# Kernel tuning notes

Measured on AMD Instinct MI355X. Metric: run time of the kernel, lower is better.

Reference implementation:

```python
import jax, jax.numpy as jnp
import numpy as np

NUM_EMBEDDINGS = 4096
EMBEDDING_DIM = 256
COMMITMENT_COST = 0.25


def setup_inputs() -> dict:
    key = jax.random.key(0)
    k1, k2 = jax.random.split(key)
    x = jax.random.normal(k1, (64, 32, 32, EMBEDDING_DIM), dtype=jnp.float32)
    # torch init: uniform(-1/K, 1/K)
    codebook = jax.random.uniform(
        k2, (NUM_EMBEDDINGS, EMBEDDING_DIM), dtype=jnp.float32,
        minval=-1.0 / NUM_EMBEDDINGS, maxval=1.0 / NUM_EMBEDDINGS)
    return {"x": x, "codebook": codebook}


def reference(x, codebook):
    D = codebook.shape[1]
    flat_x = x.reshape(-1, D)                                   # [N, D]
    distances = (jnp.sum(flat_x ** 2, axis=1, keepdims=True)
                 + jnp.sum(codebook ** 2, axis=1)
                 - 2.0 * flat_x @ codebook.T)                   # [N, K]
    encoding_indices = jnp.argmin(distances, axis=1)            # [N]
    quantized = codebook[encoding_indices].reshape(x.shape)     # gather (== one-hot matmul)
    q_sg = jax.lax.stop_gradient(quantized)
    x_sg = jax.lax.stop_gradient(x)
    commitment_loss = jnp.mean((q_sg - x) ** 2)
    codebook_loss = jnp.mean((quantized - x_sg) ** 2)
    vq_loss = codebook_loss + COMMITMENT_COST * commitment_loss
    # straight-through estimator
    quantized_st = x + jax.lax.stop_gradient(quantized - x)
    return quantized_st, vq_loss
```

## Files before the change

### kernel.cpp

```cpp
#include <hip/hip_runtime.h>
#include <stdint.h>

#define DIM     256
#define NCODES  4096
#define NROWS   65536
#define ROWS_WG 128
#define CCOLS   64
#define NCH     (NCODES / CCOLS)
#define CHB     (CCOLS * DIM)

#define OFF_BIMG  0u
#define OFF_HC    (1u << 20)

typedef __attribute__((ext_vector_type(8)))  int   i32x8;
typedef __attribute__((ext_vector_type(16))) float f32x16;
typedef const __attribute__((address_space(1))) uint32_t* gas1_t;
typedef __attribute__((address_space(3))) uint32_t*       las3_t;

__device__ __forceinline__ uint32_t pk4(float a, float b, float c, float d) {
  uint32_t lo = (uint32_t)__builtin_amdgcn_cvt_pk_fp8_f32(a, b, 0, false) & 0xFFFFu;
  uint32_t hi = (uint32_t)__builtin_amdgcn_cvt_pk_fp8_f32(c, d, 0, false) & 0xFFFFu;
  return lo | (hi << 16);
}

__global__ __launch_bounds__(256) void k1_prep(const float* __restrict__ cb,
                                               uint8_t* __restrict__ ws,
                                               float* __restrict__ out,
                                               int out_size) {
  const int t = threadIdx.x;
  if (blockIdx.x == 0 && t == 0) out[out_size - 1] = 0.0f;
  const int code = blockIdx.x * 4 + (t >> 6);
  const int l = t & 63;
  float4 v = ((const float4*)(cb + (size_t)code * DIM))[l];
  float ax = v.x * 4096.0f, ay = v.y * 4096.0f;
  float az = v.z * 4096.0f, aw = v.w * 4096.0f;
  uint32_t off = (uint32_t)(code >> 6) * (uint32_t)CHB
               + (uint32_t)(l >> 2) * 1024u
               + (uint32_t)(code & 63) * 16u + (uint32_t)(l & 3) * 4u;
  *(uint32_t*)(ws + OFF_BIMG + off) = pk4(ax, ay, az, aw);
  float s = ax * ax + ay * ay + az * az + aw * aw;
  #pragma unroll
  for (int m = 1; m < 64; m <<= 1) s += __shfl_xor(s, m, 64);
  if (l == 0) ((float*)(ws + OFF_HC))[code] = 512.0f + s * (1.0f / 8192.0f);
}

__global__ __launch_bounds__(256, 2) void k2_argmin(const float* __restrict__ x,
                                                    const float* __restrict__ cb,
                                                    uint8_t* __restrict__ ws,
                                                    float* __restrict__ out,
                                                    int out_size) {
  __shared__ uint4 smem4[4096];
  char* smem = (char*)&smem4[0];
  const int t = threadIdx.x;
  const int wave = t >> 6;
  const int lane = t & 63;
  const int c = lane & 31;
  const int g = lane >> 5;
  const int wg = blockIdx.x;
  const uint8_t* __restrict__ Bimg = ws + OFF_BIMG;
  const float* __restrict__ hcg = (const float*)(ws + OFF_HC);

  const int rbw = (wave >> 1) * 64;
  const int cbw = (wave & 1) * 32;

  const float* xb = x + (size_t)wg * ROWS_WG * DIM;
  {
    #pragma unroll
    for (int it = 0; it < 16; ++it) {
      int u = it * 256 + t;
      int row = u >> 5;
      int k8 = u & 31;
      const float4* src = (const float4*)(xb + (size_t)row * DIM + k8 * 8);
      float4 v0 = src[0], v1 = src[1];
      uint32_t* d = (uint32_t*)(smem + (k8 >> 2) * 4096 + row * 32 + (k8 & 3) * 8);
      d[0] = pk4(-v0.x, -v0.y, -v0.z, -v0.w);
      d[1] = pk4(-v1.x, -v1.y, -v1.z, -v1.w);
    }
  }
  __syncthreads();

  i32x8 a[2][4];
  #pragma unroll
  for (int rt = 0; rt < 2; ++rt)
    #pragma unroll
    for (int ks = 0; ks < 4; ++ks)
      a[rt][ks] = *(const i32x8*)(smem + (ks * 2 + g) * 4096
                                  + (rbw + rt * 32 + c) * 32);
  __syncthreads();

  char* wbuf = smem + wave * 16384;
  auto stageW = [&](int buf, int ch) {
    const uint8_t* gs = Bimg + (size_t)ch * CHB + (size_t)g * 1024
                      + (size_t)(cbw + c) * 16;
    char* lb = wbuf + buf * 8192;
    #pragma unroll
    for (int p = 0; p < 8; ++p)
      __builtin_amdgcn_global_load_lds((gas1_t)(uintptr_t)(gs + p * 2048),
                                       (las3_t)(uintptr_t)(lb + p * 1024),
                                       16, 0, 0);
  };

  uint32_t key[2][16];
  #pragma unroll
  for (int rt = 0; rt < 2; ++rt)
    #pragma unroll
    for (int r = 0; r < 16; ++r) key[rt][r] = 0xFFFFFFFFu;

  const int hoff = cbw + c;
  const uint32_t maskhi = 0xFFFFF000u;

  const int ch0 = ((wg * 7) + ((wg >> 8) * 29)) & 63;

  stageW(0, ch0);
  float h_cur = hcg[ch0 * CCOLS + hoff];

  for (int i = 0; i < NCH; ++i) {
    const int cur = i & 1;
    const int ch = (ch0 + i) & 63;
    const int chn = (ch0 + i + 1) & 63;

    const char* rb = wbuf + cur * 8192 + c * 16;
    uint4 bq[8];
    #pragma unroll
    for (int ks = 0; ks < 4; ++ks) {
      bq[ks * 2]     = *(const uint4*)(rb + (ks * 2 + g) * 1024);
      bq[ks * 2 + 1] = *(const uint4*)(rb + (ks * 2 + g) * 1024 + 512);
    }

    if (i + 1 < NCH) stageW(cur ^ 1, chn);
    float h_nxt = hcg[chn * CCOLS + hoff];

    f32x16 acc0, acc1;
    #pragma unroll
    for (int j = 0; j < 16; ++j) { acc0[j] = h_cur; acc1[j] = h_cur; }
    #pragma unroll
    for (int ks = 0; ks < 4; ++ks) {
      i32x8 b;
      b[0] = (int)bq[ks * 2].x;     b[1] = (int)bq[ks * 2].y;
      b[2] = (int)bq[ks * 2].z;     b[3] = (int)bq[ks * 2].w;
      b[4] = (int)bq[ks * 2 + 1].x; b[5] = (int)bq[ks * 2 + 1].y;
      b[6] = (int)bq[ks * 2 + 1].z; b[7] = (int)bq[ks * 2 + 1].w;
      acc0 = __builtin_amdgcn_mfma_scale_f32_32x32x64_f8f6f4(
                 a[0][ks], b, acc0, 0, 0, 0, 0x7F7F7F7F, 0, 0x7F7F7F7F);
      acc1 = __builtin_amdgcn_mfma_scale_f32_32x32x64_f8f6f4(
                 a[1][ks], b, acc1, 0, 0, 0, 0x7F7F7F7F, 0, 0x7F7F7F7F);
    }
    const uint32_t col = (uint32_t)(ch * CCOLS + hoff);
    #pragma unroll
    for (int r = 0; r < 16; ++r) {
      key[0][r] = min(key[0][r], (__float_as_uint(acc0[r]) & maskhi) | col);
      key[1][r] = min(key[1][r], (__float_as_uint(acc1[r]) & maskhi) | col);
    }
    h_cur = h_nxt;
  }

  #pragma unroll
  for (int rt = 0; rt < 2; ++rt)
    #pragma unroll
    for (int r = 0; r < 16; ++r) {
      uint32_t k = key[rt][r];
      #pragma unroll
      for (int m = 1; m < 32; m <<= 1) {
        uint32_t ko = (uint32_t)__shfl_xor((int)k, m, 32);
        k = min(k, ko);
      }
      key[rt][r] = k;
    }

  uint32_t* bk = (uint32_t*)smem;
  __syncthreads();
  if (t < 128) bk[t] = 0xFFFFFFFFu;
  __syncthreads();
  if (c == 0) {
    #pragma unroll
    for (int rt = 0; rt < 2; ++rt)
      #pragma unroll
      for (int r = 0; r < 16; ++r) {
        int rl = rbw + rt * 32 + (r & 3) + ((r >> 2) << 3) + (g << 2);
        atomicMin(&bk[rl], key[rt][r]);
      }
  }
  __syncthreads();

  float* ob = out + (size_t)wg * ROWS_WG * DIM;
  float psum = 0.0f;
  #pragma unroll 4
  for (int it = 0; it < 32; ++it) {
    int u = it * 256 + t;
    int row = u >> 6;
    int k4i = u & 63;
    int code = (int)(bk[row] & 0xFFFu);
    float4 q = ((const float4*)(cb + (size_t)code * DIM))[k4i];
    float4 xv = ((const float4*)xb)[u];
    ((float4*)ob)[u] = q;
    float dx = q.x - xv.x, dy = q.y - xv.y;
    float dz = q.z - xv.z, dw = q.w - xv.w;
    psum += dx * dx + dy * dy + dz * dz + dw * dw;
  }
  #pragma unroll
  for (int m = 1; m < 64; m <<= 1) psum += __shfl_xor(psum, m, 64);
  __shared__ float ps[4];
  if (lane == 0) ps[wave] = psum;
  __syncthreads();
  if (t == 0)
    atomicAdd(&out[out_size - 1],
              (ps[0] + ps[1] + ps[2] + ps[3]) * (1.25f / 16777216.0f));
}

extern "C" void kernel_launch(void* const* d_in, const int* in_sizes, int n_in,
                              void* d_out, int out_size, void* d_ws, size_t ws_size,
                              hipStream_t stream) {
  const float* x = (const float*)d_in[0];
  const float* cb = (const float*)d_in[1];
  uint8_t* ws = (uint8_t*)d_ws;
  float* out = (float*)d_out;

  k1_prep<<<dim3(NCODES / 4), dim3(256), 0, stream>>>(cb, ws, out, out_size);
  k2_argmin<<<dim3(NROWS / ROWS_WG), dim3(256), 0, stream>>>(x, cb, ws, out, out_size);
}
```

Measured before the change: 179.1 us.

## Share codebook chunk staging across waves and overlap argmin update with MFMA

Each wave previously staged its own copy of a codebook chunk. Now the whole workgroup cooperatively loads each 16KB chunk once into a shared, double-buffered LDS area, with __syncthreads guarding the buffer swaps. This halves LDS use and removes redundant global-to-LDS traffic. The loop is also unrolled by two with ping-pong accumulators, so the key-min reduction of the previous chunk runs alongside the MFMAs of the current chunk. The cost is two workgroup barriers per chunk pair and more live accumulator registers.

```diff
diff --git a/kernel.cpp b/kernel.cpp
--- a/kernel.cpp
+++ b/kernel.cpp
@@ -49,7 +49,7 @@
                                                     uint8_t* __restrict__ ws,
                                                     float* __restrict__ out,
                                                     int out_size) {
-  __shared__ uint4 smem4[4096];
+  __shared__ uint4 smem4[2048];
   char* smem = (char*)&smem4[0];
   const int t = threadIdx.x;
   const int wave = t >> 6;
@@ -88,15 +88,13 @@
                                   + (rbw + rt * 32 + c) * 32);
   __syncthreads();
 
-  char* wbuf = smem + wave * 16384;
-  auto stageW = [&](int buf, int ch) {
-    const uint8_t* gs = Bimg + (size_t)ch * CHB + (size_t)g * 1024
-                      + (size_t)(cbw + c) * 16;
-    char* lb = wbuf + buf * 8192;
-    #pragma unroll
-    for (int p = 0; p < 8; ++p)
-      __builtin_amdgcn_global_load_lds((gas1_t)(uintptr_t)(gs + p * 2048),
-                                       (las3_t)(uintptr_t)(lb + p * 1024),
+  auto stageB = [&](int buf, int ch) {
+    const uint8_t* gsrc = Bimg + (size_t)ch * CHB + (size_t)t * 16;
+    char* lb = smem + buf * 16384 + (t & 192) * 16;
+    #pragma unroll
+    for (int i = 0; i < 4; ++i)
+      __builtin_amdgcn_global_load_lds((gas1_t)(uintptr_t)(gsrc + i * 4096),
+                                       (las3_t)(uintptr_t)(lb + i * 4096),
                                        16, 0, 0);
   };
 
@@ -111,47 +109,94 @@
 
   const int ch0 = ((wg * 7) + ((wg >> 8) * 29)) & 63;
 
-  stageW(0, ch0);
-  float h_cur = hcg[ch0 * CCOLS + hoff];
-
-  for (int i = 0; i < NCH; ++i) {
-    const int cur = i & 1;
-    const int ch = (ch0 + i) & 63;
-    const int chn = (ch0 + i + 1) & 63;
-
-    const char* rb = wbuf + cur * 8192 + c * 16;
-    uint4 bq[8];
-    #pragma unroll
-    for (int ks = 0; ks < 4; ++ks) {
-      bq[ks * 2]     = *(const uint4*)(rb + (ks * 2 + g) * 1024);
-      bq[ks * 2 + 1] = *(const uint4*)(rb + (ks * 2 + g) * 1024 + 512);
-    }
-
-    if (i + 1 < NCH) stageW(cur ^ 1, chn);
-    float h_nxt = hcg[chn * CCOLS + hoff];
-
-    f32x16 acc0, acc1;
-    #pragma unroll
-    for (int j = 0; j < 16; ++j) { acc0[j] = h_cur; acc1[j] = h_cur; }
-    #pragma unroll
-    for (int ks = 0; ks < 4; ++ks) {
-      i32x8 b;
-      b[0] = (int)bq[ks * 2].x;     b[1] = (int)bq[ks * 2].y;
-      b[2] = (int)bq[ks * 2].z;     b[3] = (int)bq[ks * 2].w;
-      b[4] = (int)bq[ks * 2 + 1].x; b[5] = (int)bq[ks * 2 + 1].y;
-      b[6] = (int)bq[ks * 2 + 1].z; b[7] = (int)bq[ks * 2 + 1].w;
-      acc0 = __builtin_amdgcn_mfma_scale_f32_32x32x64_f8f6f4(
-                 a[0][ks], b, acc0, 0, 0, 0, 0x7F7F7F7F, 0, 0x7F7F7F7F);
-      acc1 = __builtin_amdgcn_mfma_scale_f32_32x32x64_f8f6f4(
-                 a[1][ks], b, acc1, 0, 0, 0, 0x7F7F7F7F, 0, 0x7F7F7F7F);
-    }
-    const uint32_t col = (uint32_t)(ch * CCOLS + hoff);
-    #pragma unroll
-    for (int r = 0; r < 16; ++r) {
-      key[0][r] = min(key[0][r], (__float_as_uint(acc0[r]) & maskhi) | col);
-      key[1][r] = min(key[1][r], (__float_as_uint(acc1[r]) & maskhi) | col);
-    }
-    h_cur = h_nxt;
+  stageB(0, ch0);
+  __syncthreads();
+  stageB(1, (ch0 + 1) & 63);
+
+  float hA = hcg[ch0 * CCOLS + hoff];
+  float hB = hcg[((ch0 + 1) & 63) * CCOLS + hoff];
+
+  f32x16 accA0, accA1, accB0, accB1;
+  #pragma unroll
+  for (int j = 0; j < 16; ++j) { accB0[j] = 1e30f; accB1[j] = 1e30f; }
+  uint32_t colA = 0, colB = 0;
+
+  for (int i = 0; i < NCH; i += 2) {
+    const int chA = (ch0 + i) & 63;
+    const int chB = (ch0 + i + 1) & 63;
+
+    {
+      const char* bb = smem + (cbw + c) * 16;
+      uint4 bq[8];
+      #pragma unroll
+      for (int ks = 0; ks < 4; ++ks) {
+        bq[ks * 2]     = *(const uint4*)(bb + (ks * 4 + g * 2) * 1024);
+        bq[ks * 2 + 1] = *(const uint4*)(bb + (ks * 4 + g * 2 + 1) * 1024);
+      }
+      float hA2 = hcg[((ch0 + i + 2) & 63) * CCOLS + hoff];
+      #pragma unroll
+      for (int j = 0; j < 16; ++j) { accA0[j] = hA; accA1[j] = hA; }
+      colA = (uint32_t)(chA * CCOLS + hoff);
+      #pragma unroll
+      for (int ks = 0; ks < 4; ++ks) {
+        i32x8 b;
+        b[0] = (int)bq[ks * 2].x;     b[1] = (int)bq[ks * 2].y;
+        b[2] = (int)bq[ks * 2].z;     b[3] = (int)bq[ks * 2].w;
+        b[4] = (int)bq[ks * 2 + 1].x; b[5] = (int)bq[ks * 2 + 1].y;
+        b[6] = (int)bq[ks * 2 + 1].z; b[7] = (int)bq[ks * 2 + 1].w;
+        accA0 = __builtin_amdgcn_mfma_scale_f32_32x32x64_f8f6f4(
+                    a[0][ks], b, accA0, 0, 0, 0, 0x7F7F7F7F, 0, 0x7F7F7F7F);
+        accA1 = __builtin_amdgcn_mfma_scale_f32_32x32x64_f8f6f4(
+                    a[1][ks], b, accA1, 0, 0, 0, 0x7F7F7F7F, 0, 0x7F7F7F7F);
+      }
+      #pragma unroll
+      for (int r = 0; r < 16; ++r) {
+        key[0][r] = min(key[0][r], (__float_as_uint(accB0[r]) & maskhi) | colB);
+        key[1][r] = min(key[1][r], (__float_as_uint(accB1[r]) & maskhi) | colB);
+      }
+      hA = hA2;
+    }
+    __syncthreads();
+    if (i + 2 < NCH) stageB(0, (ch0 + i + 2) & 63);
+
+    {
+      const char* bb = smem + 16384 + (cbw + c) * 16;
+      uint4 bq[8];
+      #pragma unroll
+      for (int ks = 0; ks < 4; ++ks) {
+        bq[ks * 2]     = *(const uint4*)(bb + (ks * 4 + g * 2) * 1024);
+        bq[ks * 2 + 1] = *(const uint4*)(bb + (ks * 4 + g * 2 + 1) * 1024);
+      }
+      float hB2 = hcg[((ch0 + i + 3) & 63) * CCOLS + hoff];
+      #pragma unroll
+      for (int j = 0; j < 16; ++j) { accB0[j] = hB; accB1[j] = hB; }
+      colB = (uint32_t)(chB * CCOLS + hoff);
+      #pragma unroll
+      for (int ks = 0; ks < 4; ++ks) {
+        i32x8 b;
+        b[0] = (int)bq[ks * 2].x;     b[1] = (int)bq[ks * 2].y;
+        b[2] = (int)bq[ks * 2].z;     b[3] = (int)bq[ks * 2].w;
+        b[4] = (int)bq[ks * 2 + 1].x; b[5] = (int)bq[ks * 2 + 1].y;
+        b[6] = (int)bq[ks * 2 + 1].z; b[7] = (int)bq[ks * 2 + 1].w;
+        accB0 = __builtin_amdgcn_mfma_scale_f32_32x32x64_f8f6f4(
+                    a[0][ks], b, accB0, 0, 0, 0, 0x7F7F7F7F, 0, 0x7F7F7F7F);
+        accB1 = __builtin_amdgcn_mfma_scale_f32_32x32x64_f8f6f4(
+                    a[1][ks], b, accB1, 0, 0, 0, 0x7F7F7F7F, 0, 0x7F7F7F7F);
+      }
+      #pragma unroll
+      for (int r = 0; r < 16; ++r) {
+        key[0][r] = min(key[0][r], (__float_as_uint(accA0[r]) & maskhi) | colA);
+        key[1][r] = min(key[1][r], (__float_as_uint(accA1[r]) & maskhi) | colA);
+      }
+      hB = hB2;
+    }
+    __syncthreads();
+    if (i + 3 < NCH) stageB(1, (ch0 + i + 3) & 63);
+  }
+  #pragma unroll
+  for (int r = 0; r < 16; ++r) {
+    key[0][r] = min(key[0][r], (__float_as_uint(accB0[r]) & maskhi) | colB);
+    key[1][r] = min(key[1][r], (__float_as_uint(accB1[r]) & maskhi) | colB);
   }
 
   #pragma unroll
```

Result: no change. 180.2 us (+0.6%).
